# Performance work log

Hardware: AMD Instinct MI355X
Metric: run time of the kernel (lower is better)

## Reference

```python
import math
import jax, jax.numpy as jnp
import numpy as np

B, S, D, H = 2, 2048, 1024, 16
DH = D // H
DFF = 4 * D
EPS = 1e-6
MASKED_BIAS = -10000.0


def _gelu(x):
    # GPT-2 tanh-approx GELU
    return 0.5 * x * (1.0 + jnp.tanh(math.sqrt(2.0 / math.pi) * (x + 0.044715 * x ** 3)))


def _layernorm(x, w, b):
    mean = jnp.mean(x, axis=-1, keepdims=True)
    var = jnp.mean((x - mean) ** 2, axis=-1, keepdims=True)
    return w * ((x - mean) / jnp.sqrt(var + EPS)) + b


def setup_inputs() -> dict:
    key = jax.random.key(0)
    ks = jax.random.split(key, 6)
    std = 0.02
    return {
        "hidden_states": jax.random.normal(ks[0], (B, S, D), jnp.float32),
        "w_attn": jax.random.normal(ks[1], (D, 3 * D), jnp.float32) * std,
        "b_attn": jnp.zeros((3 * D,), jnp.float32),
        "w_proj": jax.random.normal(ks[2], (D, D), jnp.float32) * std,
        "b_proj": jnp.zeros((D,), jnp.float32),
        "w_fc": jax.random.normal(ks[3], (D, DFF), jnp.float32) * std,
        "b_fc": jnp.zeros((DFF,), jnp.float32),
        "w_fc_proj": jax.random.normal(ks[4], (DFF, D), jnp.float32) * std,
        "b_fc_proj": jnp.zeros((D,), jnp.float32),
        "ln1_w": jnp.ones((D,), jnp.float32),
        "ln1_b": jnp.zeros((D,), jnp.float32),
        "ln2_w": jnp.ones((D,), jnp.float32),
        "ln2_b": jnp.zeros((D,), jnp.float32),
    }


def reference(hidden_states, w_attn, b_attn, w_proj, b_proj, w_fc, b_fc,
              w_fc_proj, b_fc_proj, ln1_w, ln1_b, ln2_w, ln2_b):
    residual = hidden_states
    x = _layernorm(hidden_states, ln1_w, ln1_b)

    # c_attn: [B,S,D] @ [D,3D] + b -> split into q,k,v
    qkv = x @ w_attn + b_attn
    q, k, v = jnp.split(qkv, 3, axis=-1)
    # split heads -> [B,H,S,DH]
    q = q.reshape(B, S, H, DH).transpose(0, 2, 1, 3)
    k = k.reshape(B, S, H, DH).transpose(0, 2, 1, 3)
    v = v.reshape(B, S, H, DH).transpose(0, 2, 1, 3)

    scores = jnp.einsum('bhqd,bhkd->bhqk', q, k) / jnp.sqrt(jnp.float32(DH))
    causal = jnp.tril(jnp.ones((S, S), bool))  # [S,S]
    scores = jnp.where(causal[None, None], scores, jnp.float32(MASKED_BIAS))
    attn = jax.nn.softmax(scores, axis=-1)
    out = jnp.einsum('bhqk,bhkd->bhqd', attn, v)
    out = out.transpose(0, 2, 1, 3).reshape(B, S, D)
    out = out @ w_proj + b_proj

    h = residual + out
    residual = h
    y = _layernorm(h, ln2_w, ln2_b)
    y = _gelu(y @ w_fc + b_fc)
    y = y @ w_fc_proj + b_fc_proj
    return residual + y
```

## Files before the change

### kernel.cpp

```cpp
#include <hip/hip_runtime.h>
#include <cstdint>
#include <cstddef>

typedef unsigned short u16;
typedef float  floatx4 __attribute__((ext_vector_type(4)));
typedef short  short8  __attribute__((ext_vector_type(8)));
typedef u16    usx4    __attribute__((ext_vector_type(4)));
typedef u16    usx8    __attribute__((ext_vector_type(8)));
typedef unsigned uintx2 __attribute__((ext_vector_type(2)));

__device__ __forceinline__ u16 f2b(float f) {
  unsigned u = __float_as_uint(f);
  unsigned r = u + 0x7fffu + ((u >> 16) & 1u);
  return (u16)(r >> 16);
}
__device__ __forceinline__ float b2f(u16 s) {
  return __uint_as_float(((unsigned)s) << 16);
}

__device__ __forceinline__ unsigned cvt_pk_bf16(float lo, float hi) {
  unsigned r;
  asm("v_cvt_pk_bf16_f32 %0, %1, %2" : "=v"(r) : "v"(lo), "v"(hi));
  return r;
}

__device__ __forceinline__ float rowmax16(float x) {
  int xi = __float_as_int(x), y;
  y = __builtin_amdgcn_update_dpp(xi, xi, 0xB1, 0xF, 0xF, false);
  x = fmaxf(x, __int_as_float(y)); xi = __float_as_int(x);
  y = __builtin_amdgcn_update_dpp(xi, xi, 0x4E, 0xF, 0xF, false);
  x = fmaxf(x, __int_as_float(y)); xi = __float_as_int(x);
  y = __builtin_amdgcn_update_dpp(xi, xi, 0x141, 0xF, 0xF, false);
  x = fmaxf(x, __int_as_float(y)); xi = __float_as_int(x);
  y = __builtin_amdgcn_update_dpp(xi, xi, 0x140, 0xF, 0xF, false);
  x = fmaxf(x, __int_as_float(y));
  return x;
}

__device__ __forceinline__ float gelu_f(float x) {
  const float k = 2.3022082f;
  float u = x * (1.0f + 0.044715f * x * x);
  float t = __builtin_amdgcn_exp2f(-k * u);
  return x * __builtin_amdgcn_rcpf(1.0f + t);
}

__device__ __forceinline__ void gl2lds16(const u16* g, u16* l) {
  __builtin_amdgcn_global_load_lds(
      (const __attribute__((address_space(1))) unsigned int*)g,
      (__attribute__((address_space(3))) unsigned int*)l, 16, 0, 0);
}

template<int N> __device__ __forceinline__ void wait_stage_barrier() {
  asm volatile("s_waitcnt vmcnt(%0)" :: "n"(N) : "memory");
  __builtin_amdgcn_s_barrier();
  __builtin_amdgcn_sched_barrier(0);
}
__device__ __forceinline__ void post_barrier() {
  __builtin_amdgcn_sched_barrier(0);
  __builtin_amdgcn_s_barrier();
  __builtin_amdgcn_sched_barrier(0);
}

#define C2SCALE 0.18033688011112042f

__global__ __launch_bounds__(256) void ln_bf16_kernel(
    const float* __restrict__ in, const float* __restrict__ w,
    const float* __restrict__ b, u16* __restrict__ out)
{
  const int row = blockIdx.x;
  const int t = threadIdx.x;
  const float* p = in + (size_t)row * 1024 + t * 4;
  floatx4 v = *(const floatx4*)p;
  float s  = v.x + v.y + v.z + v.w;
  float ss = v.x*v.x + v.y*v.y + v.z*v.z + v.w*v.w;
  #pragma unroll
  for (int m = 1; m < 64; m <<= 1) {
    s  += __shfl_xor(s,  m);
    ss += __shfl_xor(ss, m);
  }
  __shared__ float red[8];
  if ((t & 63) == 0) { red[(t >> 6)*2] = s; red[(t >> 6)*2 + 1] = ss; }
  __syncthreads();
  s  = red[0] + red[2] + red[4] + red[6];
  ss = red[1] + red[3] + red[5] + red[7];
  const float mean = s * (1.0f / 1024.0f);
  const float var  = ss * (1.0f / 1024.0f) - mean * mean;
  const float rstd = rsqrtf(var + 1e-6f);
  floatx4 wv = *(const floatx4*)(w + t * 4);
  floatx4 bv = *(const floatx4*)(b + t * 4);
  usx4 o = { f2b(wv.x * ((v.x - mean) * rstd) + bv.x),
             f2b(wv.y * ((v.y - mean) * rstd) + bv.y),
             f2b(wv.z * ((v.z - mean) * rstd) + bv.z),
             f2b(wv.w * ((v.w - mean) * rstd) + bv.w) };
  *(usx4*)(out + (size_t)row * 1024 + t * 4) = o;
}

template<int NP>
__global__ __launch_bounds__(256) void combine_ln_kernel(
    const u16* __restrict__ pp, size_t pstride,
    const float* __restrict__ res, const float* __restrict__ bias,
    const float* __restrict__ w, const float* __restrict__ b,
    float* __restrict__ hout, u16* __restrict__ yout)
{
  const int row = blockIdx.x;
  const int t = threadIdx.x;
  const size_t i0 = (size_t)row * 1024 + t * 4;
  floatx4 rv = *(const floatx4*)(res + i0);
  usx4 a[NP];
  #pragma unroll
  for (int z = 0; z < NP; ++z) a[z] = *(const usx4*)(pp + z * pstride + i0);
  floatx4 biasv = *(const floatx4*)(bias + t * 4);
  floatx4 v;
  #pragma unroll
  for (int i = 0; i < 4; ++i) {
    float acc = rv[i] + biasv[i];
    #pragma unroll
    for (int z = 0; z < NP; ++z) acc += b2f(a[z][i]);
    v[i] = acc;
  }
  *(floatx4*)(hout + i0) = v;

  float s  = v.x + v.y + v.z + v.w;
  float ss = v.x*v.x + v.y*v.y + v.z*v.z + v.w*v.w;
  #pragma unroll
  for (int m = 1; m < 64; m <<= 1) {
    s  += __shfl_xor(s,  m);
    ss += __shfl_xor(ss, m);
  }
  __shared__ float red[8];
  if ((t & 63) == 0) { red[(t >> 6)*2] = s; red[(t >> 6)*2 + 1] = ss; }
  __syncthreads();
  s  = red[0] + red[2] + red[4] + red[6];
  ss = red[1] + red[3] + red[5] + red[7];
  const float mean = s * (1.0f / 1024.0f);
  const float var  = ss * (1.0f / 1024.0f) - mean * mean;
  const float rstd = rsqrtf(var + 1e-6f);
  floatx4 wv = *(const floatx4*)(w + t * 4);
  floatx4 bv = *(const floatx4*)(b + t * 4);
  usx4 o = { f2b(wv.x * ((v.x - mean) * rstd) + bv.x),
             f2b(wv.y * ((v.y - mean) * rstd) + bv.y),
             f2b(wv.z * ((v.z - mean) * rstd) + bv.z),
             f2b(wv.w * ((v.w - mean) * rstd) + bv.w) };
  *(usx4*)(yout + i0) = o;
}

__device__ __forceinline__ void wtrans_body(
    const float* __restrict__ in, u16* __restrict__ out, int K, int N,
    int bx, int by, int tx, int ty)
{
  __shared__ u16 tile[32][33];
  const int n0 = bx * 32, k0 = by * 32;
  #pragma unroll
  for (int i = 0; i < 4; ++i)
    tile[ty + i*8][tx] = f2b(in[(size_t)(k0 + ty + i*8) * N + n0 + tx]);
  __syncthreads();
  #pragma unroll
  for (int i = 0; i < 4; ++i)
    out[(size_t)(n0 + ty + i*8) * K + k0 + tx] = tile[tx][ty + i*8];
}

__global__ __launch_bounds__(256) void wtrans4_kernel(
    const float* __restrict__ w0, const float* __restrict__ w1,
    const float* __restrict__ w2, const float* __restrict__ w3,
    u16* __restrict__ o0, u16* __restrict__ o1,
    u16* __restrict__ o2, u16* __restrict__ o3)
{
  int blk = blockIdx.x;
  const int tx = threadIdx.x & 31, ty = threadIdx.x >> 5;
  if (blk < 3072) {
    wtrans_body(w0, o0, 1024, 3072, blk % 96, blk / 96, tx, ty);
  } else if (blk < 4096) {
    blk -= 3072; wtrans_body(w1, o1, 1024, 1024, blk % 32, blk / 32, tx, ty);
  } else if (blk < 8192) {
    blk -= 4096; wtrans_body(w2, o2, 1024, 4096, blk % 128, blk / 128, tx, ty);
  } else {
    blk -= 8192; wtrans_body(w3, o3, 4096, 1024, blk % 32, blk / 32, tx, ty);
  }
}

template<int BM, int BN, int FLAGS, int MINW,
         int NX, int NY, int NZ, int RX, int RY, int RZ>
__global__ __launch_bounds__(256, MINW) void gemm_mfma_kernel(
    const u16* __restrict__ A, const u16* __restrict__ Bt,
    const float* __restrict__ bias, const float* __restrict__ Res,
    void* __restrict__ Cout, int M, int N, int K, int kLen, size_t zStride)
{
  constexpr int WM = BM / 2, WN = BN / 2;
  constexpr int MT = WM / 16, NT = WN / 16;
  constexpr int GX = NX / RX, GY = NY / RY, GZ = NZ / RZ;
  constexpr int ABUF = BM * 32, BBUF = BN * 32;
  constexpr int L = BM / 64 + BN / 64;
  __shared__ u16 As[2 * ABUF];
  __shared__ u16 Bs[2 * BBUF];

  const int lin = blockIdx.x + NX * (blockIdx.y + NY * blockIdx.z);
  const int xcd = lin & 7;
  const int idx = lin >> 3;
  const int rx = xcd % RX, ry = (xcd / RX) % RY, rz = xcd / (RX * RY);
  const int bx = rx * GX + idx % GX;
  const int by = ry * GY + (idx / GX) % GY;
  const int bz = rz * GZ + idx / (GX * GY);

  const int t = threadIdx.x;
  const int wave = t >> 6, lane = t & 63;
  const int quad = lane >> 4, l16 = lane & 15;
  const int wm = wave >> 1, wn = wave & 1;
  const int bm0 = by * BM, bn0 = bx * BN;
  const int kStart = bz * kLen;

  const int sRow = lane >> 2;
  const int sq   = (lane & 3) ^ ((lane >> 4) & 3);

  const u16* aG[BM / 64];
  u16* aL[BM / 64];
  #pragma unroll
  for (int j = 0; j < BM / 64; ++j) {
    const int band = j * 4 + wave;
    aG[j] = A + (size_t)(bm0 + band * 16 + sRow) * K + kStart + sq * 8;
    aL[j] = As + band * 512;
  }
  const u16* bG[BN / 64];
  u16* bL[BN / 64];
  #pragma unroll
  for (int j = 0; j < BN / 64; ++j) {
    const int band = j * 4 + wave;
    bG[j] = Bt + (size_t)(bn0 + band * 16 + sRow) * K + kStart + sq * 8;
    bL[j] = Bs + band * 512;
  }

  floatx4 acc[MT][NT] = {};
  const int rcol = (quad ^ (l16 >> 2)) << 3;

  auto stage = [&](int tile, int buf) {
    #pragma unroll
    for (int j = 0; j < BM / 64; ++j) gl2lds16(aG[j] + tile * 32, aL[j] + buf * ABUF);
    #pragma unroll
    for (int j = 0; j < BN / 64; ++j) gl2lds16(bG[j] + tile * 32, bL[j] + buf * BBUF);
  };
  auto compute = [&](int buf) {
    const u16* Asc = As + buf * ABUF;
    const u16* Bsc = Bs + buf * BBUF;
    short8 af[MT], bf[NT];
    #pragma unroll
    for (int mt = 0; mt < MT; ++mt)
      af[mt] = *(const short8*)&Asc[(wm*WM + mt*16 + l16) * 32 + rcol];
    #pragma unroll
    for (int nt = 0; nt < NT; ++nt)
      bf[nt] = *(const short8*)&Bsc[(wn*WN + nt*16 + l16) * 32 + rcol];
    __builtin_amdgcn_s_setprio(1);
    #pragma unroll
    for (int mt = 0; mt < MT; ++mt)
      #pragma unroll
      for (int nt = 0; nt < NT; ++nt)
        acc[mt][nt] = __builtin_amdgcn_mfma_f32_16x16x32_bf16(af[mt], bf[nt], acc[mt][nt], 0, 0, 0);
    __builtin_amdgcn_s_setprio(0);
  };

  const int nt = kLen >> 5;
  stage(0, 0);
  stage(1, 1);
  #pragma unroll 1
  for (int ti = 0; ti < nt - 2; ti += 2) {
    wait_stage_barrier<L>();
    compute(0);
    post_barrier();
    stage(ti + 2, 0);
    wait_stage_barrier<L>();
    compute(1);
    post_barrier();
    stage(ti + 3, 1);
  }
  wait_stage_barrier<L>();
  compute(0);
  wait_stage_barrier<0>();
  compute(1);

  const int orow0 = bm0 + wm * WM;
  const int ocol0 = bn0 + wn * WN;
  const size_t zoff = (size_t)bz * zStride;
  #pragma unroll
  for (int nt2 = 0; nt2 < NT; ++nt2) {
    const int col = ocol0 + nt2*16 + l16;
    const float bv = bias ? bias[col] : 0.0f;
    const float postscale = ((FLAGS & 8) && col < 1024) ? C2SCALE : 1.0f;
    #pragma unroll
    for (int mt = 0; mt < MT; ++mt) {
      #pragma unroll
      for (int r = 0; r < 4; ++r) {
        const int row = orow0 + mt*16 + quad*4 + r;
        float v = acc[mt][nt2][r] + bv;
        if (FLAGS & 1) v = gelu_f(v);
        if (FLAGS & 8) v *= postscale;
        if (FLAGS & 2) v += Res[(size_t)row * N + col];
        if (FLAGS & 4) ((u16*)Cout)[zoff + (size_t)row * N + col] = f2b(v);
        else           ((float*)Cout)[zoff + (size_t)row * N + col] = v;
      }
    }
  }
}

__global__ __launch_bounds__(256, 4) void attn_mfma_kernel(
    const u16* __restrict__ qkv, u16* __restrict__ opart, float* __restrict__ ml)
{
  __shared__ u16 Ks[64][72];
  __shared__ u16 Vt[64][72];
  __shared__ u16 Ps[64][72];

  const int t    = threadIdx.x;
  const int wave = t >> 6;
  const int lane = t & 63;
  const int quad = lane >> 4;
  const int l16  = lane & 15;
  const int pair = blockIdx.x >> 1;
  const int half = blockIdx.x & 1;
  const int h    = blockIdx.y;
  const int b    = blockIdx.z;

  const size_t base = (size_t)b * 2048 * 3072;
  const int qoff = h * 64;
  const int koff = 1024 + h * 64;
  const int voff = 2048 + h * 64;

  const int prow = t >> 2;
  const int scol = (t & 3) * 16;
  const int kmap = ((prow & 15) << 2) | (prow >> 4);
  const int kpair  = t & 31;
  const int vchunk = t >> 5;

  const size_t obase  = ((((size_t)half * 2 + b) * 16 + h) * 2048) * 64;
  const size_t mlbase = ((((size_t)half * 2 + b) * 16 + h) * 2048) * 2;

  short8 onesb;
  {
    const short v = (l16 == 0) ? (short)0x3F80 : (short)0;
    #pragma unroll
    for (int i = 0; i < 8; ++i) onesb[i] = v;
  }

  #pragma unroll 1
  for (int iter = 0; iter < 2; ++iter) {
    const int qi = iter ? (31 - pair) : pair;
    const int q0 = qi << 6;
    const int T  = qi + 1;
    const int mid = (T + 1) >> 1;
    const int t0 = half ? mid : 0;
    const int t1 = half ? T : mid;

    floatx4 of[4] = {};
    floatx4 ofl = {};
    float m[4];
    #pragma unroll
    for (int r = 0; r < 4; ++r) m[r] = -1e30f;

    if (t0 < t1) {
      __syncthreads();
      {
        const u16* qp = qkv + base + (size_t)(q0 + prow) * 3072 + qoff + scol;
        *(usx8*)&Ks[prow][scol]     = *(const usx8*)qp;
        *(usx8*)&Ks[prow][scol + 8] = *(const usx8*)(qp + 8);
      }
      __syncthreads();
      const short8 qf0 = *(const short8*)&Ks[wave*16 + l16][quad*8];
      const short8 qf1 = *(const short8*)&Ks[wave*16 + l16][32 + quad*8];

      usx8 kr0, kr1, vr0, vr1;
      {
        const int k0 = t0 << 6;
        const u16* kp = qkv + base + (size_t)(k0 + kmap) * 3072 + koff + scol;
        kr0 = *(const usx8*)kp; kr1 = *(const usx8*)(kp + 8);
        const u16* vp = qkv + base + (size_t)(k0 + 2*kpair) * 3072 + voff + vchunk*8;
        vr0 = *(const usx8*)vp; vr1 = *(const usx8*)(vp + 3072);
      }

      for (int tIdx = t0; tIdx < t1; ++tIdx) {
        __syncthreads();
        *(usx8*)&Ks[prow][scol]     = kr0;
        *(usx8*)&Ks[prow][scol + 8] = kr1;
        #pragma unroll
        for (int i = 0; i < 8; ++i)
          *(unsigned*)&Vt[vchunk*8 + i][2*kpair] =
              (unsigned)vr0[i] | ((unsigned)vr1[i] << 16);
        __syncthreads();

        if (tIdx + 1 < t1) {
          const int kn = (tIdx + 1) << 6;
          const u16* kp = qkv + base + (size_t)(kn + kmap) * 3072 + koff + scol;
          kr0 = *(const usx8*)kp; kr1 = *(const usx8*)(kp + 8);
          const u16* vp = qkv + base + (size_t)(kn + 2*kpair) * 3072 + voff + vchunk*8;
          vr0 = *(const usx8*)vp; vr1 = *(const usx8*)(vp + 3072);
        }

        const int k0 = tIdx << 6;
        floatx4 sf[4];
        #pragma unroll
        for (int kt = 0; kt < 4; ++kt) {
          short8 kf0 = *(const short8*)&Ks[kt*16 + l16][quad*8];
          short8 kf1 = *(const short8*)&Ks[kt*16 + l16][32 + quad*8];
          floatx4 z = {};
          z      = __builtin_amdgcn_mfma_f32_16x16x32_bf16(qf0, kf0, z, 0, 0, 0);
          sf[kt] = __builtin_amdgcn_mfma_f32_16x16x32_bf16(qf1, kf1, z, 0, 0, 0);
        }

        const bool diag = (tIdx == qi);
        #pragma unroll
        for (int r = 0; r < 4; ++r) {
          float sv0 = sf[0][r], sv1 = sf[1][r], sv2 = sf[2][r], sv3 = sf[3][r];
          if (diag) {
            const int qrow = q0 + wave*16 + quad*4 + r;
            const int kbase = k0 + 4*l16;
            if (kbase     > qrow) sv0 = -1e30f;
            if (kbase + 1 > qrow) sv1 = -1e30f;
            if (kbase + 2 > qrow) sv2 = -1e30f;
            if (kbase + 3 > qrow) sv3 = -1e30f;
          }
          float mx = fmaxf(fmaxf(sv0, sv1), fmaxf(sv2, sv3));
          mx = rowmax16(mx);
          const float nm = fmaxf(m[r], mx);
          const float alpha = __builtin_amdgcn_exp2f(m[r] - nm);
          m[r] = nm;
          const float p0 = __builtin_amdgcn_exp2f(sv0 - nm);
          const float p1 = __builtin_amdgcn_exp2f(sv1 - nm);
          const float p2 = __builtin_amdgcn_exp2f(sv2 - nm);
          const float p3 = __builtin_amdgcn_exp2f(sv3 - nm);
          uintx2 pw = { cvt_pk_bf16(p0, p1), cvt_pk_bf16(p2, p3) };
          *(uintx2*)&Ps[wave*16 + quad*4 + r][l16 * 4] = pw;
          #pragma unroll
          for (int dht = 0; dht < 4; ++dht) of[dht][r] *= alpha;
          ofl[r] *= alpha;
        }

        short8 pf0 = *(const short8*)&Ps[wave*16 + l16][quad*8];
        short8 pf1 = *(const short8*)&Ps[wave*16 + l16][32 + quad*8];
        #pragma unroll
        for (int dht = 0; dht < 4; ++dht) {
          short8 vf0 = *(const short8*)&Vt[dht*16 + l16][quad*8];
          short8 vf1 = *(const short8*)&Vt[dht*16 + l16][32 + quad*8];
          of[dht] = __builtin_amdgcn_mfma_f32_16x16x32_bf16(pf0, vf0, of[dht], 0, 0, 0);
          of[dht] = __builtin_amdgcn_mfma_f32_16x16x32_bf16(pf1, vf1, of[dht], 0, 0, 0);
        }
        ofl = __builtin_amdgcn_mfma_f32_16x16x32_bf16(pf0, onesb, ofl, 0, 0, 0);
        ofl = __builtin_amdgcn_mfma_f32_16x16x32_bf16(pf1, onesb, ofl, 0, 0, 0);
      }
    }

    #pragma unroll
    for (int r = 0; r < 4; ++r) {
      const int s = q0 + wave*16 + quad*4 + r;
      u16* orow = opart + obase + (size_t)s * 64;
      #pragma unroll
      for (int dht = 0; dht < 4; ++dht) orow[dht*16 + l16] = f2b(of[dht][r]);
      const float lr = __shfl(ofl[r], quad * 16);
      if (l16 == 0) { ml[mlbase + 2*s] = m[r]; ml[mlbase + 2*s + 1] = lr; }
    }
  }
}

__global__ __launch_bounds__(256) void attn_combine_kernel(
    const u16* __restrict__ opart, const float* __restrict__ ml,
    u16* __restrict__ out)
{
  const int t = threadIdx.x;
  const int s = blockIdx.x * 4 + (t >> 6);
  const int lane = t & 63;
  const int h = blockIdx.y, b = blockIdx.z;

  const size_t o0  = ((((size_t)0 * 2 + b) * 16 + h) * 2048 + s) * 64 + lane;
  const size_t o1  = ((((size_t)1 * 2 + b) * 16 + h) * 2048 + s) * 64 + lane;
  const size_t ml0 = ((((size_t)0 * 2 + b) * 16 + h) * 2048 + s) * 2;
  const size_t ml1 = ((((size_t)1 * 2 + b) * 16 + h) * 2048 + s) * 2;

  const float m0 = ml[ml0], l0 = ml[ml0 + 1];
  const float m1 = ml[ml1], l1 = ml[ml1 + 1];
  const float M  = fmaxf(m0, m1);
  const float w0 = __builtin_amdgcn_exp2f(m0 - M);
  const float w1 = __builtin_amdgcn_exp2f(m1 - M);
  const float L  = w0 * l0 + w1 * l1;
  const float o  = w0 * b2f(opart[o0]) + w1 * b2f(opart[o1]);
  out[((size_t)b * 2048 + s) * 1024 + h * 64 + lane] = f2b(o / L);
}

template<int NP>
__global__ __launch_bounds__(256) void ksplit_combine_kernel(
    const u16* __restrict__ pp, size_t pstride,
    const float* __restrict__ res, const float* __restrict__ bias,
    float* __restrict__ out)
{
  const size_t i0 = ((size_t)blockIdx.x * 256 + threadIdx.x) * 8;
  usx8 a[NP];
  #pragma unroll
  for (int z = 0; z < NP; ++z) a[z] = *(const usx8*)(pp + z * pstride + i0);
  const int col = (int)(i0 & 1023);
  floatx4 bv0 = *(const floatx4*)(bias + col);
  floatx4 bv1 = *(const floatx4*)(bias + col + 4);
  floatx4 h0 = *(const floatx4*)(res + i0);
  floatx4 h1 = *(const floatx4*)(res + i0 + 4);
  floatx4 o0, o1;
  #pragma unroll
  for (int i = 0; i < 4; ++i) {
    float s0 = h0[i] + bv0[i], s1 = h1[i] + bv1[i];
    #pragma unroll
    for (int z = 0; z < NP; ++z) { s0 += b2f(a[z][i]); s1 += b2f(a[z][4+i]); }
    o0[i] = s0; o1[i] = s1;
  }
  *(floatx4*)(out + i0)     = o0;
  *(floatx4*)(out + i0 + 4) = o1;
}

extern "C" void kernel_launch(void* const* d_in, const int* in_sizes, int n_in,
                              void* d_out, int out_size, void* d_ws, size_t ws_size,
                              hipStream_t stream) {
  const float* hidden    = (const float*)d_in[0];
  const float* w_attn    = (const float*)d_in[1];
  const float* b_attn    = (const float*)d_in[2];
  const float* w_proj    = (const float*)d_in[3];
  const float* b_proj    = (const float*)d_in[4];
  const float* w_fc      = (const float*)d_in[5];
  const float* b_fc      = (const float*)d_in[6];
  const float* w_fc_proj = (const float*)d_in[7];
  const float* b_fc_proj = (const float*)d_in[8];
  const float* ln1_w     = (const float*)d_in[9];
  const float* ln1_b     = (const float*)d_in[10];
  const float* ln2_w     = (const float*)d_in[11];
  const float* ln2_b     = (const float*)d_in[12];

  char* wsb = (char*)d_ws;
  u16*   qkvb  = (u16*)  (wsb + (size_t)( 0u << 20));
  u16*   xb    = (u16*)  (wsb + (size_t)(24u << 20));
  u16*   opart = (u16*)  (wsb + (size_t)(24u << 20));
  float* mlbuf = (float*)(wsb + (size_t)(40u << 20));
  u16*   attnb = (u16*)  (wsb + (size_t)(42u << 20));
  u16*   wqT   = (u16*)  (wsb + (size_t)(50u << 20));
  u16*   wpT   = (u16*)  (wsb + (size_t)(56u << 20));
  u16*   wfT   = (u16*)  (wsb + (size_t)(58u << 20));
  u16*   wfpT  = (u16*)  (wsb + (size_t)(66u << 20));
  u16*   pproj = (u16*)  (wsb + (size_t)(24u << 20));
  float* hbuf  = (float*)(wsb + (size_t)(42u << 20));
  u16*   yb    = (u16*)  (wsb + (size_t)( 0u << 20));
  u16*   fcb   = (u16*)  (wsb + (size_t)( 8u << 20));
  u16*   p4    = (u16*)  (wsb + (size_t)(74u << 20));
  u16*   pfcp0 = (u16*)  (wsb + (size_t)( 0u << 20));
  const size_t zstr8  = ((size_t)8u << 20) / 2;
  const size_t zstr58 = ((size_t)58u << 20) / 2;

  const bool big = ws_size >= ((size_t)106u << 20);

  wtrans4_kernel<<<dim3(12288), 256, 0, stream>>>(
      w_attn, w_proj, w_fc, w_fc_proj, wqT, wpT, wfT, wfpT);

  ln_bf16_kernel<<<4096, 256, 0, stream>>>(hidden, ln1_w, ln1_b, xb);
  gemm_mfma_kernel<128,128,12,4, 24,32,1, 2,4,1><<<dim3(24, 32, 1), 256, 0, stream>>>(
      xb, wqT, b_attn, nullptr, qkvb, 4096, 3072, 1024, 1024, 0);
  attn_mfma_kernel<<<dim3(32, 16, 2), 256, 0, stream>>>(qkvb, opart, mlbuf);
  attn_combine_kernel<<<dim3(512, 16, 2), 256, 0, stream>>>(opart, mlbuf, attnb);

  if (big) {
    gemm_mfma_kernel<128,128,4,4, 8,32,4, 1,2,4><<<dim3(8, 32, 4), 256, 0, stream>>>(
        attnb, wpT, nullptr, nullptr, p4, 4096, 1024, 1024, 256, zstr8);
    combine_ln_kernel<4><<<4096, 256, 0, stream>>>(
        p4, zstr8, hidden, b_proj, ln2_w, ln2_b, hbuf, yb);
  } else {
    gemm_mfma_kernel<128,64,4,4, 16,32,2, 1,4,2><<<dim3(16, 32, 2), 256, 0, stream>>>(
        attnb, wpT, nullptr, nullptr, pproj, 4096, 1024, 1024, 512, zstr8);
    combine_ln_kernel<2><<<4096, 256, 0, stream>>>(
        pproj, zstr8, hidden, b_proj, ln2_w, ln2_b, hbuf, yb);
  }
  gemm_mfma_kernel<128,128,5,4, 32,32,1, 2,4,1><<<dim3(32, 32, 1), 256, 0, stream>>>(
      yb, wfT, b_fc, nullptr, fcb, 4096, 4096, 1024, 1024, 0);
  if (big) {
    gemm_mfma_kernel<128,128,4,4, 8,32,4, 1,2,4><<<dim3(8, 32, 4), 256, 0, stream>>>(
        fcb, wfpT, nullptr, nullptr, p4, 4096, 1024, 4096, 1024, zstr8);
    ksplit_combine_kernel<4><<<dim3(2048), 256, 0, stream>>>(
        p4, zstr8, hbuf, b_fc_proj, (float*)d_out);
  } else {
    gemm_mfma_kernel<128,64,4,4, 16,32,2, 1,4,2><<<dim3(16, 32, 2), 256, 0, stream>>>(
        fcb, wfpT, nullptr, nullptr, pfcp0, 4096, 1024, 4096, 2048, zstr58);
    ksplit_combine_kernel<2><<<dim3(2048), 256, 0, stream>>>(
        pfcp0, zstr58, hbuf, b_fc_proj, (float*)d_out);
  }
}
```

Before: 355.2 us.

## Replace 128x128 GEMM with 256x256 tile, 8-wave, half-tile interleaved prefetch kernel

Swaps the 4-wave 128x128 bf16 MFMA GEMM for a 512-thread 256x256 tile kernel with a 64-wide K step. The K step is split into sub-stages where A and B half-slices are prefetched between MFMA blocks, with a new LDS swizzle. The goal is more operand reuse per loaded byte and better overlap of loads with MFMA work. In exchange, grids become much smaller (as few as 192-256 blocks on a 256-CU part) and register pressure rises, which risks poor occupancy and tail imbalance.

```diff
diff --git a/kernel.cpp b/kernel.cpp
--- a/kernel.cpp
+++ b/kernel.cpp
@@ -52,11 +52,6 @@
 
 template<int N> __device__ __forceinline__ void wait_stage_barrier() {
   asm volatile("s_waitcnt vmcnt(%0)" :: "n"(N) : "memory");
-  __builtin_amdgcn_s_barrier();
-  __builtin_amdgcn_sched_barrier(0);
-}
-__device__ __forceinline__ void post_barrier() {
-  __builtin_amdgcn_sched_barrier(0);
   __builtin_amdgcn_s_barrier();
   __builtin_amdgcn_sched_barrier(0);
 }
@@ -178,20 +173,16 @@
   }
 }
 
-template<int BM, int BN, int FLAGS, int MINW,
-         int NX, int NY, int NZ, int RX, int RY, int RZ>
-__global__ __launch_bounds__(256, MINW) void gemm_mfma_kernel(
+template<int FLAGS, int NX, int NY, int NZ, int RX, int RY, int RZ>
+__global__ __launch_bounds__(512, 2) void gemm256_kernel(
     const u16* __restrict__ A, const u16* __restrict__ Bt,
-    const float* __restrict__ bias, const float* __restrict__ Res,
+    const float* __restrict__ bias,
     void* __restrict__ Cout, int M, int N, int K, int kLen, size_t zStride)
 {
-  constexpr int WM = BM / 2, WN = BN / 2;
-  constexpr int MT = WM / 16, NT = WN / 16;
+  constexpr int SLOT = 256 * 32;
   constexpr int GX = NX / RX, GY = NY / RY, GZ = NZ / RZ;
-  constexpr int ABUF = BM * 32, BBUF = BN * 32;
-  constexpr int L = BM / 64 + BN / 64;
-  __shared__ u16 As[2 * ABUF];
-  __shared__ u16 Bs[2 * BBUF];
+  __shared__ u16 As[2][2][SLOT];
+  __shared__ u16 Bs[2][2][SLOT];
 
   const int lin = blockIdx.x + NX * (blockIdx.y + NY * blockIdx.z);
   const int xcd = lin & 7;
@@ -202,96 +193,134 @@
   const int bz = rz * GZ + idx / (GX * GY);
 
   const int t = threadIdx.x;
-  const int wave = t >> 6, lane = t & 63;
+  const int wave = t >> 6;
+  const int lane = t & 63;
   const int quad = lane >> 4, l16 = lane & 15;
-  const int wm = wave >> 1, wn = wave & 1;
-  const int bm0 = by * BM, bn0 = bx * BN;
+  const int wm = wave >> 2;
+  const int wn = wave & 3;
+  const int bm0 = by * 256, bn0 = bx * 256;
   const int kStart = bz * kLen;
 
   const int sRow = lane >> 2;
-  const int sq   = (lane & 3) ^ ((lane >> 4) & 3);
-
-  const u16* aG[BM / 64];
-  u16* aL[BM / 64];
-  #pragma unroll
-  for (int j = 0; j < BM / 64; ++j) {
-    const int band = j * 4 + wave;
-    aG[j] = A + (size_t)(bm0 + band * 16 + sRow) * K + kStart + sq * 8;
-    aL[j] = As + band * 512;
-  }
-  const u16* bG[BN / 64];
-  u16* bL[BN / 64];
-  #pragma unroll
-  for (int j = 0; j < BN / 64; ++j) {
-    const int band = j * 4 + wave;
-    bG[j] = Bt + (size_t)(bn0 + band * 16 + sRow) * K + kStart + sq * 8;
-    bL[j] = Bs + band * 512;
-  }
-
-  floatx4 acc[MT][NT] = {};
-  const int rcol = (quad ^ (l16 >> 2)) << 3;
-
-  auto stage = [&](int tile, int buf) {
-    #pragma unroll
-    for (int j = 0; j < BM / 64; ++j) gl2lds16(aG[j] + tile * 32, aL[j] + buf * ABUF);
-    #pragma unroll
-    for (int j = 0; j < BN / 64; ++j) gl2lds16(bG[j] + tile * 32, bL[j] + buf * BBUF);
+  const int sq   = (lane & 3) ^ ((lane >> 3) & 3);
+
+  const u16* aGb[2]; const u16* bGb[2];
+  #pragma unroll
+  for (int j = 0; j < 2; ++j) {
+    const int band = wave * 2 + j;
+    aGb[j] = A  + (size_t)(bm0 + band * 16 + sRow) * K + kStart + sq * 8;
+    bGb[j] = Bt + (size_t)(bn0 + band * 16 + sRow) * K + kStart + sq * 8;
+  }
+
+  auto stageA = [&](int kt, int kk) {
+    u16* dst = &As[kt & 1][kk][0];
+    #pragma unroll
+    for (int j = 0; j < 2; ++j)
+      gl2lds16(aGb[j] + kt * 64 + kk * 32, dst + (wave * 2 + j) * 512);
   };
-  auto compute = [&](int buf) {
-    const u16* Asc = As + buf * ABUF;
-    const u16* Bsc = Bs + buf * BBUF;
-    short8 af[MT], bf[NT];
-    #pragma unroll
-    for (int mt = 0; mt < MT; ++mt)
-      af[mt] = *(const short8*)&Asc[(wm*WM + mt*16 + l16) * 32 + rcol];
-    #pragma unroll
-    for (int nt = 0; nt < NT; ++nt)
-      bf[nt] = *(const short8*)&Bsc[(wn*WN + nt*16 + l16) * 32 + rcol];
+  auto stageB = [&](int kt, int kk) {
+    u16* dst = &Bs[kt & 1][kk][0];
+    #pragma unroll
+    for (int j = 0; j < 2; ++j)
+      gl2lds16(bGb[j] + kt * 64 + kk * 32, dst + (wave * 2 + j) * 512);
+  };
+
+  floatx4 acc[8][4] = {};
+  const int rcol = (quad ^ ((l16 >> 1) & 3)) << 3;
+
+  const int NT = kLen >> 6;
+  stageA(0, 0); stageB(0, 0); stageA(0, 1); stageB(0, 1);
+
+  #pragma unroll 1
+  for (int kt = 0; kt < NT; ++kt) {
+    const int buf = kt & 1;
+    const bool pf = (kt + 1 < NT);
+    short8 af[4], bf[4];
+
+    wait_stage_barrier<4>();
+    #pragma unroll
+    for (int nt2 = 0; nt2 < 4; ++nt2)
+      bf[nt2] = *(const short8*)&Bs[buf][0][(wn*64 + nt2*16 + l16) * 32 + rcol];
+    #pragma unroll
+    for (int mt = 0; mt < 4; ++mt)
+      af[mt] = *(const short8*)&As[buf][0][(wm*128 + mt*16 + l16) * 32 + rcol];
+    if (pf) stageA(kt + 1, 0);
+    __builtin_amdgcn_s_barrier();
+    asm volatile("s_waitcnt lgkmcnt(0)" ::: "memory");
+    __builtin_amdgcn_sched_barrier(0);
     __builtin_amdgcn_s_setprio(1);
     #pragma unroll
-    for (int mt = 0; mt < MT; ++mt)
+    for (int mt = 0; mt < 4; ++mt)
       #pragma unroll
-      for (int nt = 0; nt < NT; ++nt)
-        acc[mt][nt] = __builtin_amdgcn_mfma_f32_16x16x32_bf16(af[mt], bf[nt], acc[mt][nt], 0, 0, 0);
+      for (int nt2 = 0; nt2 < 4; ++nt2)
+        acc[mt][nt2] = __builtin_amdgcn_mfma_f32_16x16x32_bf16(af[mt], bf[nt2], acc[mt][nt2], 0, 0, 0);
     __builtin_amdgcn_s_setprio(0);
-  };
-
-  const int nt = kLen >> 5;
-  stage(0, 0);
-  stage(1, 1);
-  #pragma unroll 1
-  for (int ti = 0; ti < nt - 2; ti += 2) {
-    wait_stage_barrier<L>();
-    compute(0);
-    post_barrier();
-    stage(ti + 2, 0);
-    wait_stage_barrier<L>();
-    compute(1);
-    post_barrier();
-    stage(ti + 3, 1);
-  }
-  wait_stage_barrier<L>();
-  compute(0);
-  wait_stage_barrier<0>();
-  compute(1);
-
-  const int orow0 = bm0 + wm * WM;
-  const int ocol0 = bn0 + wn * WN;
+    __builtin_amdgcn_s_barrier();
+    #pragma unroll
+    for (int mt = 0; mt < 4; ++mt)
+      af[mt] = *(const short8*)&As[buf][0][(wm*128 + (mt+4)*16 + l16) * 32 + rcol];
+    if (pf) stageB(kt + 1, 0);
+    __builtin_amdgcn_s_barrier();
+    asm volatile("s_waitcnt lgkmcnt(0)" ::: "memory");
+    __builtin_amdgcn_sched_barrier(0);
+    __builtin_amdgcn_s_setprio(1);
+    #pragma unroll
+    for (int mt = 0; mt < 4; ++mt)
+      #pragma unroll
+      for (int nt2 = 0; nt2 < 4; ++nt2)
+        acc[mt+4][nt2] = __builtin_amdgcn_mfma_f32_16x16x32_bf16(af[mt], bf[nt2], acc[mt+4][nt2], 0, 0, 0);
+    __builtin_amdgcn_s_setprio(0);
+    if (pf) wait_stage_barrier<4>(); else wait_stage_barrier<0>();
+    #pragma unroll
+    for (int nt2 = 0; nt2 < 4; ++nt2)
+      bf[nt2] = *(const short8*)&Bs[buf][1][(wn*64 + nt2*16 + l16) * 32 + rcol];
+    #pragma unroll
+    for (int mt = 0; mt < 4; ++mt)
+      af[mt] = *(const short8*)&As[buf][1][(wm*128 + mt*16 + l16) * 32 + rcol];
+    if (pf) stageA(kt + 1, 1);
+    __builtin_amdgcn_s_barrier();
+    asm volatile("s_waitcnt lgkmcnt(0)" ::: "memory");
+    __builtin_amdgcn_sched_barrier(0);
+    __builtin_amdgcn_s_setprio(1);
+    #pragma unroll
+    for (int mt = 0; mt < 4; ++mt)
+      #pragma unroll
+      for (int nt2 = 0; nt2 < 4; ++nt2)
+        acc[mt][nt2] = __builtin_amdgcn_mfma_f32_16x16x32_bf16(af[mt], bf[nt2], acc[mt][nt2], 0, 0, 0);
+    __builtin_amdgcn_s_setprio(0);
+    __builtin_amdgcn_s_barrier();
+    #pragma unroll
+    for (int mt = 0; mt < 4; ++mt)
+      af[mt] = *(const short8*)&As[buf][1][(wm*128 + (mt+4)*16 + l16) * 32 + rcol];
+    if (pf) stageB(kt + 1, 1);
+    __builtin_amdgcn_s_barrier();
+    asm volatile("s_waitcnt lgkmcnt(0)" ::: "memory");
+    __builtin_amdgcn_sched_barrier(0);
+    __builtin_amdgcn_s_setprio(1);
+    #pragma unroll
+    for (int mt = 0; mt < 4; ++mt)
+      #pragma unroll
+      for (int nt2 = 0; nt2 < 4; ++nt2)
+        acc[mt+4][nt2] = __builtin_amdgcn_mfma_f32_16x16x32_bf16(af[mt], bf[nt2], acc[mt+4][nt2], 0, 0, 0);
+    __builtin_amdgcn_s_setprio(0);
+  }
+
+  const int orow0 = bm0 + wm * 128;
+  const int ocol0 = bn0 + wn * 64;
   const size_t zoff = (size_t)bz * zStride;
   #pragma unroll
-  for (int nt2 = 0; nt2 < NT; ++nt2) {
+  for (int nt2 = 0; nt2 < 4; ++nt2) {
     const int col = ocol0 + nt2*16 + l16;
     const float bv = bias ? bias[col] : 0.0f;
     const float postscale = ((FLAGS & 8) && col < 1024) ? C2SCALE : 1.0f;
     #pragma unroll
-    for (int mt = 0; mt < MT; ++mt) {
+    for (int mt = 0; mt < 8; ++mt) {
       #pragma unroll
       for (int r = 0; r < 4; ++r) {
         const int row = orow0 + mt*16 + quad*4 + r;
         float v = acc[mt][nt2][r] + bv;
         if (FLAGS & 1) v = gelu_f(v);
         if (FLAGS & 8) v *= postscale;
-        if (FLAGS & 2) v += Res[(size_t)row * N + col];
         if (FLAGS & 4) ((u16*)Cout)[zoff + (size_t)row * N + col] = f2b(v);
         else           ((float*)Cout)[zoff + (size_t)row * N + col] = v;
       }
@@ -548,32 +577,32 @@
       w_attn, w_proj, w_fc, w_fc_proj, wqT, wpT, wfT, wfpT);
 
   ln_bf16_kernel<<<4096, 256, 0, stream>>>(hidden, ln1_w, ln1_b, xb);
-  gemm_mfma_kernel<128,128,12,4, 24,32,1, 2,4,1><<<dim3(24, 32, 1), 256, 0, stream>>>(
-      xb, wqT, b_attn, nullptr, qkvb, 4096, 3072, 1024, 1024, 0);
+  gemm256_kernel<12, 12,16,1, 2,4,1><<<dim3(12, 16, 1), 512, 0, stream>>>(
+      xb, wqT, b_attn, qkvb, 4096, 3072, 1024, 1024, 0);
   attn_mfma_kernel<<<dim3(32, 16, 2), 256, 0, stream>>>(qkvb, opart, mlbuf);
   attn_combine_kernel<<<dim3(512, 16, 2), 256, 0, stream>>>(opart, mlbuf, attnb);
 
   if (big) {
-    gemm_mfma_kernel<128,128,4,4, 8,32,4, 1,2,4><<<dim3(8, 32, 4), 256, 0, stream>>>(
-        attnb, wpT, nullptr, nullptr, p4, 4096, 1024, 1024, 256, zstr8);
+    gemm256_kernel<4, 4,16,4, 1,2,4><<<dim3(4, 16, 4), 512, 0, stream>>>(
+        attnb, wpT, nullptr, p4, 4096, 1024, 1024, 256, zstr8);
     combine_ln_kernel<4><<<4096, 256, 0, stream>>>(
         p4, zstr8, hidden, b_proj, ln2_w, ln2_b, hbuf, yb);
   } else {
-    gemm_mfma_kernel<128,64,4,4, 16,32,2, 1,4,2><<<dim3(16, 32, 2), 256, 0, stream>>>(
-        attnb, wpT, nullptr, nullptr, pproj, 4096, 1024, 1024, 512, zstr8);
+    gemm256_kernel<4, 4,16,2, 1,4,2><<<dim3(4, 16, 2), 512, 0, stream>>>(
+        attnb, wpT, nullptr, pproj, 4096, 1024, 1024, 512, zstr8);
     combine_ln_kernel<2><<<4096, 256, 0, stream>>>(
         pproj, zstr8, hidden, b_proj, ln2_w, ln2_b, hbuf, yb);
   }
-  gemm_mfma_kernel<128,128,5,4, 32,32,1, 2,4,1><<<dim3(32, 32, 1), 256, 0, stream>>>(
-      yb, wfT, b_fc, nullptr, fcb, 4096, 4096, 1024, 1024, 0);
+  gemm256_kernel<5, 16,16,1, 2,4,1><<<dim3(16, 16, 1), 512, 0, stream>>>(
+      yb, wfT, b_fc, fcb, 4096, 4096, 1024, 1024, 0);
   if (big) {
-    gemm_mfma_kernel<128,128,4,4, 8,32,4, 1,2,4><<<dim3(8, 32, 4), 256, 0, stream>>>(
-        fcb, wfpT, nullptr, nullptr, p4, 4096, 1024, 4096, 1024, zstr8);
+    gemm256_kernel<4, 4,16,4, 1,2,4><<<dim3(4, 16, 4), 512, 0, stream>>>(
+        fcb, wfpT, nullptr, p4, 4096, 1024, 4096, 1024, zstr8);
     ksplit_combine_kernel<4><<<dim3(2048), 256, 0, stream>>>(
         p4, zstr8, hbuf, b_fc_proj, (float*)d_out);
   } else {
-    gemm_mfma_kernel<128,64,4,4, 16,32,2, 1,4,2><<<dim3(16, 32, 2), 256, 0, stream>>>(
-        fcb, wfpT, nullptr, nullptr, pfcp0, 4096, 1024, 4096, 2048, zstr58);
+    gemm256_kernel<4, 4,16,2, 1,4,2><<<dim3(4, 16, 2), 512, 0, stream>>>(
+        fcb, wfpT, nullptr, pfcp0, 4096, 1024, 4096, 2048, zstr58);
     ksplit_combine_kernel<2><<<dim3(2048), 256, 0, stream>>>(
         pfcp0, zstr58, hbuf, b_fc_proj, (float*)d_out);
   }
```

Measured after the change: 358.1 us. Within noise of the previous version (+0.8%).
